# Kernel optimization log

Hardware: AMD Instinct MI355X
Metric: run time of the kernel (lower is better)

Reference implementation:

```python
import jax, jax.numpy as jnp
import numpy as np

TEMPERATURE = 0.5
EPS = 1e-8  # torch CosineSimilarity eps


def setup_inputs() -> dict:
    key = jax.random.key(0)
    k1, k2 = jax.random.split(key)
    return {
        "z_i": jax.random.normal(k1, (4096, 256), dtype=jnp.float32),
        "z_j": jax.random.normal(k2, (4096, 256), dtype=jnp.float32),
    }


def _nt_xent(z_i, z_j):
    B = z_i.shape[0]          # full_batch_size (world_size == 1)
    N = 2 * B
    z = jnp.concatenate([z_i, z_j], axis=0)              # [N, D]
    norm = jnp.maximum(jnp.linalg.norm(z, axis=1, keepdims=True), EPS)
    zn = z / norm
    # cosine similarity matrix via one GEMM (instead of broadcast O(N^2*D) materialization)
    sim = (zn @ zn.T) / TEMPERATURE                      # [N, N]
    # positive pairs: diag offsets +B and -B
    pos = jnp.concatenate([jnp.diagonal(sim, B), jnp.diagonal(sim, -B)])  # [N]
    # CE with logits = [pos, negatives(row excluding self & positive)] and label 0:
    # loss_row = -pos + logsumexp([pos] + negs) = -pos + logsumexp(row excluding self-diagonal)
    sim_masked = jnp.where(jnp.eye(N, dtype=bool), -jnp.inf, sim)
    lse = jax.nn.logsumexp(sim_masked, axis=1)           # [N]
    return jnp.sum(lse - pos) / N


def reference(z_i, z_j):
    return _nt_xent(z_i, z_j)
```

## Files before the change

### kernel.cpp

```cpp
#include <hip/hip_runtime.h>
#include <hip/hip_bf16.h>
#include <hip/hip_fp8.h>

#define N_TOT 8192
#define DIM 256
#define HALF_B 4096
#define NCHUNK 32
#define NPAIR (NCHUNK * (NCHUNK + 1) / 2)
#define NBLK (NPAIR * 4)
#define TILE_COLS 32
#define NTILES 4
#define NSLOT 128
#define LSE_BLOCKS (N_TOT / 4)
#define KEXP 2.8853900817779268f
#define TILE_BYTES (TILE_COLS * DIM)

typedef __attribute__((ext_vector_type(4))) float facc;
typedef __attribute__((ext_vector_type(2))) long long lpair;

typedef __attribute__((address_space(1))) const unsigned int guint;
typedef __attribute__((address_space(3))) unsigned int luint;

static __device__ __forceinline__ void gload16(const void* g, void* l) {
    __builtin_amdgcn_global_load_lds((guint*)g, (luint*)l, 16, 0, 0);
}
static __device__ __forceinline__ unsigned char f2fp8(float x) {
    __hip_fp8_e4m3 h(x);
    return (unsigned char)h.__x;
}
static __device__ __forceinline__ float fp82f(unsigned char b) {
    __hip_fp8_e4m3 h; h.__x = (__hip_fp8_storage_t)b;
    return (float)h;
}
static __device__ __forceinline__ float fast_exp2(float x) {
#if __has_builtin(__builtin_amdgcn_exp2f)
    return __builtin_amdgcn_exp2f(x);
#else
    return exp2f(x);
#endif
}
static __device__ __forceinline__ facc mfma8(long long a, long long b, facc c) {
    return __builtin_amdgcn_mfma_f32_16x16x32_fp8_fp8(a, b, c, 0, 0, 0);
}

__global__ __launch_bounds__(256) void norm_kernel(const float* __restrict__ zi,
                                                   const float* __restrict__ zj,
                                                   unsigned char* __restrict__ znP) {
    int row  = blockIdx.x * 4 + (threadIdx.x >> 6);
    int lane = threadIdx.x & 63;
    const float* src = (row < HALF_B) ? (zi + (size_t)row * DIM)
                                      : (zj + (size_t)(row - HALF_B) * DIM);
    float4 v = reinterpret_cast<const float4*>(src)[lane];
    float ss = v.x * v.x + v.y * v.y + v.z * v.z + v.w * v.w;
    #pragma unroll
    for (int off = 32; off; off >>= 1) ss += __shfl_xor(ss, off);
    float inv = 1.0f / fmaxf(sqrtf(ss), 1e-8f);
    uchar4 o;
    o.x = f2fp8(v.x * inv);
    o.y = f2fp8(v.y * inv);
    o.z = f2fp8(v.z * inv);
    o.w = f2fp8(v.w * inv);
    int b = lane * 4;
    int g = b >> 3;
    int pb = ((((g & 3) << 3) | (g >> 2)) << 3) | (b & 7);
    *reinterpret_cast<uchar4*>(znP + (size_t)row * DIM + pb) = o;
}

__global__ __launch_bounds__(256, 4) void sim_kernel(const unsigned char* __restrict__ znP,
                                                     float* __restrict__ partial) {
    __shared__ __align__(16) unsigned char smem[2 * TILE_BYTES];
    __shared__ float colred[4][128];
    const int lane = threadIdx.x & 63;
    const int wv   = threadIdx.x >> 6;
    const int lrow = lane & 15;
    const int kq   = lane >> 4;

    const int pairId = blockIdx.x >> 2;
    const int h      = blockIdx.x & 1;
    const int g      = (blockIdx.x >> 1) & 1;
    int i = 0, rem = pairId;
    while (rem >= NCHUNK - i) { rem -= NCHUNK - i; ++i; }
    const int j = i + rem;
    const int rowBase  = i * 256 + g * 128 + wv * 32;
    const int colStart = j * 256 + h * 128;

    int srcOff[2];
    #pragma unroll
    for (int q = 0; q < 2; ++q) {
        int c  = (wv * 2 + q) * 64 + lane;
        int r  = c >> 4;
        int cc = c & 15;
        srcOff[q] = r * DIM + ((cc ^ (r & 15)) << 4);
    }
    const unsigned char* znPC = znP + (size_t)colStart * DIM;

#define STAGE(buf, ct) do {                                                   \
        const unsigned char* gsb = znPC + (size_t)(ct) * TILE_BYTES;          \
        _Pragma("unroll")                                                     \
        for (int q = 0; q < 2; ++q)                                           \
            gload16(gsb + srcOff[q],                                          \
                    smem + (buf) * TILE_BYTES + (wv * 2 + q) * 1024);         \
    } while (0)

    STAGE(0, 0);

    lpair a[2][4];
    #pragma unroll
    for (int t = 0; t < 2; ++t)
        #pragma unroll
        for (int s = 0; s < 4; ++s)
            a[t][s] = *reinterpret_cast<const lpair*>(
                znP + (size_t)(rowBase + t * 16 + lrow) * DIM + kq * 64 + s * 16);
    #pragma unroll
    for (int t = 0; t < 2; ++t)
        #pragma unroll
        for (int s = 0; s < 4; ++s)
            asm volatile("" : "+v"(a[t][s]));

    float rowsum[2][4];
    #pragma unroll
    for (int t = 0; t < 2; ++t)
        #pragma unroll
        for (int jj = 0; jj < 4; ++jj) rowsum[t][jj] = 0.0f;

    colred[wv][lane]      = 0.0f;
    colred[wv][lane + 64] = 0.0f;

    __syncthreads();

    #pragma unroll 1
    for (int tile = 0; tile < NTILES; ++tile) {
        const int cur = tile & 1;
        if (tile + 1 < NTILES) STAGE(cur ^ 1, tile + 1);

        #pragma unroll
        for (int cs = 0; cs < 2; ++cs) {
            const unsigned char* base =
                smem + cur * TILE_BYTES + (cs * 16 + lrow) * DIM;
            facc acc[2];
            acc[0] = (facc){0.f, 0.f, 0.f, 0.f};
            acc[1] = (facc){0.f, 0.f, 0.f, 0.f};
            #pragma unroll
            for (int s = 0; s < 4; ++s) {
                lpair bv = *reinterpret_cast<const lpair*>(
                    base + (((kq * 4 + s) ^ lrow) << 4));
                #pragma unroll
                for (int t = 0; t < 2; ++t) {
                    acc[t] = mfma8(a[t][s][0], bv[0], acc[t]);
                    acc[t] = mfma8(a[t][s][1], bv[1], acc[t]);
                }
            }

            const int colBase = colStart + tile * TILE_COLS + cs * 16;
            float csum = 0.0f;
            #pragma unroll
            for (int t = 0; t < 2; ++t) {
                const int tRowBase = rowBase + t * 16;
                if (colBase == tRowBase) {
                    #pragma unroll
                    for (int jj = 0; jj < 4; ++jj) {
                        float e = fast_exp2(acc[t][jj] * KEXP);
                        if (lrow == kq * 4 + jj) e = 0.0f;
                        rowsum[t][jj] += e;
                        csum += e;
                    }
                } else {
                    #pragma unroll
                    for (int jj = 0; jj < 4; ++jj) {
                        float e = fast_exp2(acc[t][jj] * KEXP);
                        rowsum[t][jj] += e;
                        csum += e;
                    }
                }
            }
            csum += __shfl_xor(csum, 16);
            csum += __shfl_xor(csum, 32);
            if (kq == 0)
                colred[wv][tile * TILE_COLS + cs * 16 + lrow] += csum;
        }
        __syncthreads();
    }
#undef STAGE

    const int slotR = j * 2 + h;
    #pragma unroll
    for (int t = 0; t < 2; ++t)
        #pragma unroll
        for (int jj = 0; jj < 4; ++jj) {
            float v = rowsum[t][jj];
            v += __shfl_xor(v, 1);
            v += __shfl_xor(v, 2);
            v += __shfl_xor(v, 4);
            v += __shfl_xor(v, 8);
            if (lrow == 0)
                partial[(size_t)slotR * N_TOT + rowBase + t * 16 + kq * 4 + jj] = v;
        }

    if (i != j && threadIdx.x < 128) {
        int c = threadIdx.x;
        float s = colred[0][c] + colred[1][c] + colred[2][c] + colred[3][c];
        partial[(size_t)(64 + 2 * i + g) * N_TOT + colStart + c] = s;
    }
}

__global__ __launch_bounds__(256) void lse_kernel(const unsigned char* __restrict__ znP,
                                                  const float* __restrict__ partial,
                                                  float* __restrict__ blockSums) {
    const int lane = threadIdx.x & 63;
    const int wv   = threadIdx.x >> 6;
    const int r    = blockIdx.x * 4 + wv;
    const int rb   = r >> 8;
    const int rp   = r ^ HALF_B;
    uchar4 va = *reinterpret_cast<const uchar4*>(znP + (size_t)r  * DIM + lane * 4);
    uchar4 vb = *reinterpret_cast<const uchar4*>(znP + (size_t)rp * DIM + lane * 4);
    float d = fp82f(va.x) * fp82f(vb.x) + fp82f(va.y) * fp82f(vb.y) +
              fp82f(va.z) * fp82f(vb.z) + fp82f(va.w) * fp82f(vb.w);
    float S = 0.0f;
    if (lane >= 2 * rb) S += partial[(size_t)lane * N_TOT + r];
    if (lane < 2 * rb)  S += partial[(size_t)(64 + lane) * N_TOT + r];
    #pragma unroll
    for (int off = 32; off; off >>= 1) {
        d += __shfl_xor(d, off);
        S += __shfl_xor(S, off);
    }
    __shared__ float red[4];
    if (lane == 0) red[wv] = logf(S) - d * 2.0f;
    __syncthreads();
    if (threadIdx.x == 0)
        blockSums[blockIdx.x] = red[0] + red[1] + red[2] + red[3];
}

__global__ __launch_bounds__(256) void final_kernel(const float* __restrict__ bs,
                                                    float* __restrict__ out) {
    int t = threadIdx.x;
    float v = 0.0f;
    #pragma unroll
    for (int q = 0; q < LSE_BLOCKS / 256; ++q) v += bs[t + q * 256];
    #pragma unroll
    for (int off = 32; off; off >>= 1) v += __shfl_xor(v, off);
    __shared__ float red[4];
    if ((t & 63) == 0) red[t >> 6] = v;
    __syncthreads();
    if (t == 0) out[0] = (red[0] + red[1] + red[2] + red[3]) / (float)N_TOT;
}

extern "C" void kernel_launch(void* const* d_in, const int* in_sizes, int n_in,
                              void* d_out, int out_size, void* d_ws, size_t ws_size,
                              hipStream_t stream) {
    const float* zi = (const float*)d_in[0];
    const float* zj = (const float*)d_in[1];
    char* ws = (char*)d_ws;

    unsigned char* znP = (unsigned char*)ws;
    float* partial    = (float*)(znP + (size_t)N_TOT * DIM);
    float* blockSums  = partial + (size_t)NSLOT * N_TOT;
    float* out        = (float*)d_out;

    norm_kernel<<<N_TOT / 4, 256, 0, stream>>>(zi, zj, znP);
    sim_kernel<<<NBLK, 256, 0, stream>>>(znP, partial);
    lse_kernel<<<LSE_BLOCKS, 256, 0, stream>>>(znP, partial, blockSums);
    final_kernel<<<1, 256, 0, stream>>>(blockSums, out);
}
```

Before: 40.44 us.

## Capture positive-pair logits in sim kernel and transpose partial-sum layout

The sim kernel now writes the positive-pair similarity directly from the MFMA accumulator when a tile lies on the +B diagonal. This removes the separate FP8 dot product in the LSE kernel. The partial-sum buffer is transposed to row-major [row][slot], so each LSE wave reads one contiguous float2 per lane instead of 64 strided loads. The cost is scattered strided stores of partials in the sim kernel and an extra branch in its hot loop.

```diff
diff --git a/kernel.cpp b/kernel.cpp
--- a/kernel.cpp
+++ b/kernel.cpp
@@ -28,10 +28,6 @@
     __hip_fp8_e4m3 h(x);
     return (unsigned char)h.__x;
 }
-static __device__ __forceinline__ float fp82f(unsigned char b) {
-    __hip_fp8_e4m3 h; h.__x = (__hip_fp8_storage_t)b;
-    return (float)h;
-}
 static __device__ __forceinline__ float fast_exp2(float x) {
 #if __has_builtin(__builtin_amdgcn_exp2f)
     return __builtin_amdgcn_exp2f(x);
@@ -67,7 +63,8 @@
 }
 
 __global__ __launch_bounds__(256, 4) void sim_kernel(const unsigned char* __restrict__ znP,
-                                                     float* __restrict__ partial) {
+                                                     float* __restrict__ partial,
+                                                     float* __restrict__ pos) {
     __shared__ __align__(16) unsigned char smem[2 * TILE_BYTES];
     __shared__ float colred[4][128];
     const int lane = threadIdx.x & 63;
@@ -163,6 +160,19 @@
                         if (lrow == kq * 4 + jj) e = 0.0f;
                         rowsum[t][jj] += e;
                         csum += e;
+                    }
+                } else if (colBase == tRowBase + HALF_B) {
+                    #pragma unroll
+                    for (int jj = 0; jj < 4; ++jj) {
+                        float e = fast_exp2(acc[t][jj] * KEXP);
+                        rowsum[t][jj] += e;
+                        csum += e;
+                        if (lrow == kq * 4 + jj) {
+                            int r = tRowBase + lrow;
+                            float p = acc[t][jj] * 2.0f;
+                            pos[r]          = p;
+                            pos[r + HALF_B] = p;
+                        }
                     }
                 } else {
                     #pragma unroll
@@ -182,7 +192,7 @@
     }
 #undef STAGE
 
-    const int slotR = j * 2 + h;
+    const int offR = (j * 2 + h) * 2;
     #pragma unroll
     for (int t = 0; t < 2; ++t)
         #pragma unroll
@@ -193,38 +203,29 @@
             v += __shfl_xor(v, 4);
             v += __shfl_xor(v, 8);
             if (lrow == 0)
-                partial[(size_t)slotR * N_TOT + rowBase + t * 16 + kq * 4 + jj] = v;
+                partial[(size_t)(rowBase + t * 16 + kq * 4 + jj) * NSLOT + offR] = v;
         }
 
     if (i != j && threadIdx.x < 128) {
         int c = threadIdx.x;
         float s = colred[0][c] + colred[1][c] + colred[2][c] + colred[3][c];
-        partial[(size_t)(64 + 2 * i + g) * N_TOT + colStart + c] = s;
+        partial[(size_t)(colStart + c) * NSLOT + (2 * i + g) * 2 + 1] = s;
     }
 }
 
-__global__ __launch_bounds__(256) void lse_kernel(const unsigned char* __restrict__ znP,
-                                                  const float* __restrict__ partial,
+__global__ __launch_bounds__(256) void lse_kernel(const float* __restrict__ partial,
+                                                  const float* __restrict__ pos,
                                                   float* __restrict__ blockSums) {
     const int lane = threadIdx.x & 63;
     const int wv   = threadIdx.x >> 6;
     const int r    = blockIdx.x * 4 + wv;
     const int rb   = r >> 8;
-    const int rp   = r ^ HALF_B;
-    uchar4 va = *reinterpret_cast<const uchar4*>(znP + (size_t)r  * DIM + lane * 4);
-    uchar4 vb = *reinterpret_cast<const uchar4*>(znP + (size_t)rp * DIM + lane * 4);
-    float d = fp82f(va.x) * fp82f(vb.x) + fp82f(va.y) * fp82f(vb.y) +
-              fp82f(va.z) * fp82f(vb.z) + fp82f(va.w) * fp82f(vb.w);
-    float S = 0.0f;
-    if (lane >= 2 * rb) S += partial[(size_t)lane * N_TOT + r];
-    if (lane < 2 * rb)  S += partial[(size_t)(64 + lane) * N_TOT + r];
-    #pragma unroll
-    for (int off = 32; off; off >>= 1) {
-        d += __shfl_xor(d, off);
-        S += __shfl_xor(S, off);
-    }
+    float2 v = reinterpret_cast<const float2*>(partial + (size_t)r * NSLOT)[lane];
+    float S = (lane >= 2 * rb) ? v.x : v.y;
+    #pragma unroll
+    for (int off = 32; off; off >>= 1) S += __shfl_xor(S, off);
     __shared__ float red[4];
-    if (lane == 0) red[wv] = logf(S) - d * 2.0f;
+    if (lane == 0) red[wv] = logf(S) - pos[r];
     __syncthreads();
     if (threadIdx.x == 0)
         blockSums[blockIdx.x] = red[0] + red[1] + red[2] + red[3];
@@ -252,12 +253,13 @@
     char* ws = (char*)d_ws;
 
     unsigned char* znP = (unsigned char*)ws;
-    float* partial    = (float*)(znP + (size_t)N_TOT * DIM);
-    float* blockSums  = partial + (size_t)NSLOT * N_TOT;
+    float* pos        = (float*)(znP + (size_t)N_TOT * DIM);
+    float* partial    = pos + N_TOT;
+    float* blockSums  = partial + (size_t)N_TOT * NSLOT;
     float* out        = (float*)d_out;
 
     norm_kernel<<<N_TOT / 4, 256, 0, stream>>>(zi, zj, znP);
-    sim_kernel<<<NBLK, 256, 0, stream>>>(znP, partial);
-    lse_kernel<<<LSE_BLOCKS, 256, 0, stream>>>(znP, partial, blockSums);
+    sim_kernel<<<NBLK, 256, 0, stream>>>(znP, partial, pos);
+    lse_kernel<<<LSE_BLOCKS, 256, 0, stream>>>(partial, pos, blockSums);
     final_kernel<<<1, 256, 0, stream>>>(blockSums, out);
 }
```

After: 38.73 us. 1.04x faster.
